# Optimization experiments

Measured on AMD Instinct MI355X. Metric: run time of the kernel, lower is better.

## Reference

```python
import jax, jax.numpy as jnp
import numpy as np

D_MODEL = 1024
HEAD_DIM = 64
NUM_HEADS = 16
NUM_KV_HEADS = 4
LOGIT_CAP = 50.0
F_EMBED = 10000


def rope(inputs, positions, head_dim, max_wavelength):
    # inputs: [B, T, N, H]; positions: [B, T]
    fraction = 2.0 * jnp.arange(head_dim // 2, dtype=jnp.float32) / head_dim
    timescale = max_wavelength ** fraction  # [H/2]
    sinusoid = positions.astype(jnp.float32)[..., None] / timescale  # [B, T, H/2]
    sinusoid = sinusoid[..., None, :]  # [B, T, 1, H/2]
    sin, cos = jnp.sin(sinusoid), jnp.cos(sinusoid)
    first, second = jnp.split(inputs, 2, axis=-1)
    return jnp.concatenate([first * cos - second * sin,
                            second * cos + first * sin], axis=-1)


def setup_inputs() -> dict:
    key = jax.random.key(0)
    kx, kq, kkv, ko = jax.random.split(key, 4)
    B, T = 1, 2048
    x = jax.random.normal(kx, (B, T, D_MODEL), dtype=jnp.float32)
    pos = jnp.broadcast_to(jnp.arange(T, dtype=jnp.int32)[None, :], (B, T))
    # mask semantics: True == masked out (logit set to -100). Causal: disallow s > t.
    mask = jnp.broadcast_to(jnp.triu(jnp.ones((T, T), dtype=bool), k=1)[None], (B, T, T))
    sq = 1.0 / np.sqrt(D_MODEL)
    wq = jax.random.normal(kq, (NUM_HEADS, D_MODEL, HEAD_DIM), dtype=jnp.float32) * sq
    wkv = jax.random.normal(kkv, (2, NUM_KV_HEADS, D_MODEL, HEAD_DIM), dtype=jnp.float32) * sq
    wout = jax.random.normal(ko, (NUM_HEADS, HEAD_DIM, D_MODEL), dtype=jnp.float32) * sq
    return {"x": x, "pos": pos, "mask": mask, "wq": wq, "wkv": wkv, "wout": wout}


def reference(x, pos, mask, wq, wkv, wout):
    B, T, _ = x.shape
    K, G = NUM_KV_HEADS, NUM_HEADS // NUM_KV_HEADS
    # projections
    q = jnp.einsum('BTD,NDH->BTNH', x, wq)  # [B,T,N,H]
    q = rope(q, pos, HEAD_DIM, F_EMBED) / jnp.sqrt(jnp.float32(HEAD_DIM))
    kv = jnp.einsum('BSD,CKDH->CBSKH', x, wkv)  # [2,B,S,K,H]
    k_proj, v_proj = kv[0], kv[1]
    k_proj = rope(k_proj, pos, HEAD_DIM, F_EMBED)
    # grouped logits
    qg = q.reshape(B, T, K, G, HEAD_DIM)
    logits = jnp.einsum('BTKGH,BSKH->BTKGS', qg, k_proj).reshape(B, T, NUM_HEADS, T)
    # soft-cap + mask (True in mask => masked => -100)
    logits = jnp.tanh(logits / LOGIT_CAP) * LOGIT_CAP
    logits = jnp.where(~mask[:, :, None, :], logits, -100.0)
    probs = jax.nn.softmax(logits, axis=-1).astype(k_proj.dtype)
    # grouped outer
    pg = probs.reshape(B, T, K, G, T)
    enc = jnp.einsum('BTKGS,BSKH->BTKGH', pg, v_proj).reshape(B, T, NUM_HEADS, HEAD_DIM)
    return jnp.einsum('BTNH,NHD->BTD', enc, wout)
```

## Files before the change

### kernel.cpp

```cpp
#include <hip/hip_runtime.h>
#include <hip/hip_bf16.h>
#include <cstdint>

#define T_SEQ 2048
#define DM    1024
#define HD    64
#define NH    16
#define NKV   4

typedef __attribute__((ext_vector_type(8))) short short8;
typedef __attribute__((ext_vector_type(4))) short short4v;
typedef __attribute__((ext_vector_type(4))) float f32x4;

__device__ __forceinline__ unsigned short f2bf(float f) {
    union { float f; unsigned u; } v; v.f = f;
    unsigned r = v.u + 0x7FFF + ((v.u >> 16) & 1);
    return (unsigned short)(r >> 16);
}

__global__ __launch_bounds__(256) void prep_kernel(const float* __restrict__ x,
                                                   const int* __restrict__ pos,
                                                   const float* __restrict__ wq,
                                                   const float* __restrict__ wkv,
                                                   const float* __restrict__ wout,
                                                   unsigned short* __restrict__ xb,
                                                   float2* __restrict__ stab,
                                                   unsigned short* __restrict__ wqkvT,
                                                   unsigned short* __restrict__ woutT) {
    __shared__ unsigned short tile[64][65];
    int bid = blockIdx.x;
    if (bid < 2048) {
        int i = bid * 256 + threadIdx.x;
        f32x4 v = *(const f32x4*)(x + i * 4);
        short4v o;
        #pragma unroll
        for (int j = 0; j < 4; j++) o[j] = (short)f2bf(v[j]);
        *(short4v*)(xb + i * 4) = o;
        if (i < 65536) {
            int tt = i >> 5, hm = i & 31;
            float ang = (float)pos[tt] * exp2f((float)hm * -0.41524101186092029f);
            float sv, cv;
            sincosf(ang, &sv, &cv);
            stab[i] = make_float2(sv, cv);
        }
    } else {
        int bid2 = bid - 2048;
        int d0 = (bid2 & 15) * 64;
        int bz = bid2 >> 4;
        int tc = threadIdx.x & 63, tr = threadIdx.x >> 6;
        if (bz < 24) {
            const float* src = (bz < 16) ? (wq + bz * 65536) : (wkv + (bz - 16) * 65536);
            #pragma unroll
            for (int rr = 0; rr < 64; rr += 4)
                tile[rr + tr][tc] = f2bf(src[(d0 + rr + tr) * 64 + tc]);
            __syncthreads();
            #pragma unroll
            for (int rr = 0; rr < 64; rr += 4)
                wqkvT[(bz * 64 + rr + tr) * 1024 + d0 + tc] = tile[tc][rr + tr];
        } else {
            int j0 = (bz - 24) * 64;
            #pragma unroll
            for (int rr = 0; rr < 64; rr += 4)
                tile[rr + tr][tc] = f2bf(wout[(j0 + rr + tr) * 1024 + d0 + tc]);
            __syncthreads();
            #pragma unroll
            for (int rr = 0; rr < 64; rr += 4)
                woutT[(d0 + rr + tr) * 1024 + j0 + tc] = tile[tc][rr + tr];
        }
    }
}

__global__ __launch_bounds__(256) void gemm_qkv(const unsigned short* __restrict__ A,
                                                const unsigned short* __restrict__ Bt,
                                                const float2* __restrict__ stab,
                                                unsigned short* __restrict__ qb,
                                                unsigned short* __restrict__ kb2,
                                                unsigned short* __restrict__ vT) {
    __shared__ __align__(16) unsigned char smem[33280];
    unsigned short (*lA)[4096] = (unsigned short (*)[4096])smem;
    unsigned short (*lB)[2048] = (unsigned short (*)[2048])(smem + 16384);
    float (*etile)[65] = (float (*)[65])smem;

    int wid = threadIdx.x >> 6;
    int lane = threadIdx.x & 63;
    int l15 = lane & 15, g = lane >> 4;
    int wr = wid >> 1, wc = wid & 1;
    int r0 = blockIdx.x * 128;
    int by = blockIdx.y;
    int c0 = by * 64;

    f32x4 acc[4][2];
    #pragma unroll
    for (int m = 0; m < 4; m++)
        #pragma unroll
        for (int n = 0; n < 2; n++)
            acc[m][n] = (f32x4){0.f, 0.f, 0.f, 0.f};

    auto stage = [&](int buf, int k0) {
        #pragma unroll
        for (int i = 0; i < 2; i++) {
            int off = i * 4096 + threadIdx.x * 16;
            const unsigned short* gpa = A + (r0 + (off >> 6)) * DM + k0 + ((off & 63) >> 1);
            __builtin_amdgcn_global_load_lds(
                (const __attribute__((address_space(1))) unsigned int*)gpa,
                (__attribute__((address_space(3))) unsigned int*)&lA[buf][off >> 1], 16, 0, 0);
        }
        int off = threadIdx.x * 16;
        const unsigned short* gpb = Bt + (c0 + (off >> 6)) * DM + k0 + ((off & 63) >> 1);
        __builtin_amdgcn_global_load_lds(
            (const __attribute__((address_space(1))) unsigned int*)gpb,
            (__attribute__((address_space(3))) unsigned int*)&lB[buf][off >> 1], 16, 0, 0);
    };

    stage(0, 0);
    __syncthreads();
    for (int k0 = 0; k0 < DM; k0 += 32) {
        int buf = (k0 >> 5) & 1;
        if (k0 + 32 < DM) stage(buf ^ 1, k0 + 32);
        short8 af[4], bfr[2];
        #pragma unroll
        for (int m = 0; m < 4; m++)
            af[m] = *(const short8*)&lA[buf][(wr * 64 + m * 16 + l15) * 32 + g * 8];
        #pragma unroll
        for (int n = 0; n < 2; n++)
            bfr[n] = *(const short8*)&lB[buf][(wc * 32 + n * 16 + l15) * 32 + g * 8];
        #pragma unroll
        for (int m = 0; m < 4; m++)
            #pragma unroll
            for (int n = 0; n < 2; n++)
                acc[m][n] = __builtin_amdgcn_mfma_f32_16x16x32_bf16(af[m], bfr[n], acc[m][n], 0, 0, 0);
        __syncthreads();
    }

    #pragma unroll
    for (int m = 0; m < 4; m++)
        #pragma unroll
        for (int n = 0; n < 2; n++)
            #pragma unroll
            for (int rr = 0; rr < 4; rr++)
                etile[wr * 64 + m * 16 + g * 4 + rr][wc * 32 + n * 16 + l15] = acc[m][n][rr];
    __syncthreads();

    if (by < 20) {
        #pragma unroll
        for (int rh = 0; rh < 2; rh++) {
            int row = threadIdx.x >> 2;
            int h0 = (threadIdx.x & 3) * 16;
            int t = r0 + rh * 64 + row;
            float res[16];
            #pragma unroll
            for (int j = 0; j < 16; j++) {
                int h = h0 + j;
                float val = etile[rh * 64 + row][h];
                float oth = etile[rh * 64 + row][h ^ 32];
                float2 sc = stab[t * 32 + (h & 31)];
                res[j] = (h < 32) ? (val * sc.y - oth * sc.x) : (val * sc.y + oth * sc.x);
            }
            if (by < 16) {
                short8 o[2];
                #pragma unroll
                for (int j = 0; j < 16; j++) o[j >> 3][j & 7] = (short)f2bf(res[j] * 0.125f);
                unsigned short* qrow = qb + t * 1024 + by * 64 + h0;
                *(short8*)qrow = o[0];
                *(short8*)(qrow + 8) = o[1];
            } else {
                int kvh = by - 16;
                int swz = (t & 7) << 3;
                short8 o[2];
                #pragma unroll
                for (int j = 0; j < 16; j++) o[j >> 3][j & 7] = (short)f2bf(res[j]);
                unsigned short* krow = kb2 + kvh * (T_SEQ * 64) + t * 64;
                *(short8*)(krow + (h0 ^ swz)) = o[0];
                *(short8*)(krow + ((h0 + 8) ^ swz)) = o[1];
            }
        }
    } else {
        int cgl = threadIdx.x >> 2;
        int u0 = (threadIdx.x & 3) * 16;
        int cglob = (by - 20) * 64 + cgl;
        int cx = cgl & 7;
        #pragma unroll
        for (int rh = 0; rh < 2; rh++) {
            short8 o[2];
            #pragma unroll
            for (int j = 0; j < 16; j++) {
                int u = u0 + j;
                int chunk = u >> 3, qin = u & 7;
                int hi = qin >> 2, r = qin & 3;
                int sg = chunk ^ cx;
                int tl = (sg >> 2) * 32 + hi * 16 + (sg & 3) * 4 + r;
                o[j >> 3][j & 7] = (short)f2bf(etile[rh * 64 + tl][cgl]);
            }
            unsigned short* vrow = vT + cglob * 2048 + r0 + rh * 64 + u0;
            *(short8*)vrow = o[0];
            *(short8*)(vrow + 8) = o[1];
        }
    }
}

template<int BM, int BN>
__global__ __launch_bounds__(256) void gemm_lds(const unsigned short* __restrict__ A,
                                                const unsigned short* __restrict__ Bt,
                                                float* __restrict__ C,
                                                int K, int lda, int ldb, int ldc) {
    constexpr int MR = BM / 32;
    constexpr int NC = BN / 32;
    __shared__ unsigned short lA[2][BM * 32];
    __shared__ unsigned short lB[2][BN * 32];

    int wid = threadIdx.x >> 6;
    int lane = threadIdx.x & 63;
    int l15 = lane & 15, g = lane >> 4;
    int wr = wid >> 1, wc = wid & 1;
    int r0 = blockIdx.x * BM;
    int c0 = blockIdx.y * BN;

    f32x4 acc[MR][NC];
    #pragma unroll
    for (int m = 0; m < MR; m++)
        #pragma unroll
        for (int n = 0; n < NC; n++)
            acc[m][n] = (f32x4){0.f, 0.f, 0.f, 0.f};

    auto stage = [&](int buf, int k0) {
        #pragma unroll
        for (int i = 0; i < BM / 64; i++) {
            int off = i * 4096 + threadIdx.x * 16;
            const unsigned short* gp = A + (r0 + (off >> 6)) * lda + k0 + ((off & 63) >> 1);
            __builtin_amdgcn_global_load_lds(
                (const __attribute__((address_space(1))) unsigned int*)gp,
                (__attribute__((address_space(3))) unsigned int*)&lA[buf][off >> 1], 16, 0, 0);
        }
        #pragma unroll
        for (int i = 0; i < (BN + 63) / 64; i++) {
            int off = i * 4096 + threadIdx.x * 16;
            if (off < BN * 64) {
                const unsigned short* gp = Bt + (c0 + (off >> 6)) * ldb + k0 + ((off & 63) >> 1);
                __builtin_amdgcn_global_load_lds(
                    (const __attribute__((address_space(1))) unsigned int*)gp,
                    (__attribute__((address_space(3))) unsigned int*)&lB[buf][off >> 1], 16, 0, 0);
            }
        }
    };

    stage(0, 0);
    __syncthreads();
    for (int k0 = 0; k0 < K; k0 += 32) {
        int buf = (k0 >> 5) & 1;
        if (k0 + 32 < K) stage(buf ^ 1, k0 + 32);
        short8 af[MR], bfr[NC];
        #pragma unroll
        for (int m = 0; m < MR; m++)
            af[m] = *(const short8*)&lA[buf][(wr * (BM / 2) + m * 16 + l15) * 32 + g * 8];
        #pragma unroll
        for (int n = 0; n < NC; n++)
            bfr[n] = *(const short8*)&lB[buf][(wc * (BN / 2) + n * 16 + l15) * 32 + g * 8];
        #pragma unroll
        for (int m = 0; m < MR; m++)
            #pragma unroll
            for (int n = 0; n < NC; n++)
                acc[m][n] = __builtin_amdgcn_mfma_f32_16x16x32_bf16(af[m], bfr[n], acc[m][n], 0, 0, 0);
        __syncthreads();
    }
    #pragma unroll
    for (int m = 0; m < MR; m++) {
        int row = r0 + wr * (BM / 2) + m * 16 + g * 4;
        #pragma unroll
        for (int n = 0; n < NC; n++) {
            int col = c0 + wc * (BN / 2) + n * 16 + l15;
            #pragma unroll
            for (int rr = 0; rr < 4; rr++)
                C[(row + rr) * ldc + col] = acc[m][n][rr];
        }
    }
}

__global__ __launch_bounds__(512, 4) void attn_kernel(const unsigned short* __restrict__ qb,
                                                      const unsigned short* __restrict__ kb2,
                                                      const unsigned short* __restrict__ vT,
                                                      unsigned short* __restrict__ enc) {
    __shared__ unsigned short lk[2][8192];
    __shared__ unsigned short lv[2][8192];
    __shared__ float s_lc[3][4][16];

    int v = blockIdx.x;
    int kvh = blockIdx.y;
    int hp = blockIdx.z;
    int wid = threadIdx.x >> 6;
    int lane = threadIdx.x & 63;
    int l15 = lane & 15, g = lane >> 4;
    int half = wid >> 2;
    int c = wid & 3;
    int qt = half ? v : (127 - v);
    int q0 = qt * 16;
    int t = q0 + l15;
    int head0 = kvh * 4 + hp * 2;

    short8 qf0[2], qf1[2];
    #pragma unroll
    for (int e = 0; e < 2; e++) {
        const unsigned short* qrow = qb + t * 1024 + (head0 + e) * 64;
        qf0[e] = *(const short8*)(qrow + g * 8);
        qf1[e] = *(const short8*)(qrow + 32 + g * 8);
    }

    f32x4 acc[2][4];
    #pragma unroll
    for (int e = 0; e < 2; e++)
        #pragma unroll
        for (int ht = 0; ht < 4; ht++)
            acc[e][ht] = (f32x4){0.f, 0.f, 0.f, 0.f};
    float lrun[2] = {0.f, 0.f};
    int nph = (127 - v) / 8 + 1;

    auto stage = [&](int buf, int s0) {
        #pragma unroll
        for (int i = 0; i < 4; i++) {
            if (wid < 4) {
                int seg = wid * 4 + i;
                const unsigned short* gp = kb2 + kvh * (T_SEQ * 64) + s0 * 64 + seg * 512 + lane * 8;
                __builtin_amdgcn_global_load_lds(
                    (const __attribute__((address_space(1))) unsigned int*)gp,
                    (__attribute__((address_space(3))) unsigned int*)&lk[buf][seg * 512], 16, 0, 0);
            } else {
                int sv = (wid - 4) * 4 + i;
                int h = sv * 4 + (lane >> 4);
                const unsigned short* gp = vT + (kvh * 64 + h) * T_SEQ + s0 + (lane & 15) * 8;
                __builtin_amdgcn_global_load_lds(
                    (const __attribute__((address_space(1))) unsigned int*)gp,
                    (__attribute__((address_space(3))) unsigned int*)&lv[buf][sv * 512], 16, 0, 0);
            }
        }
    };

    stage(0, 0);
    __syncthreads();

    for (int ph = 0; ph < nph; ph++) {
        int buf = ph & 1;
        if (ph + 1 < nph) stage(buf ^ 1, (ph + 1) * 128);
        int s0c = ph * 128 + c * 32;
        if (s0c <= q0 + 15) {
            bool needmask = (s0c + 31 > q0);
            union PU { short8 s8; unsigned w[4]; } pf[2];
            #pragma unroll
            for (int u = 0; u < 2; u++) {
                int srow = c * 32 + u * 16 + l15;
                int swz = (srow & 7) << 3;
                short8 kf0 = *(const short8*)(&lk[buf][srow * 64 + ((g * 8) ^ swz)]);
                short8 kf1 = *(const short8*)(&lk[buf][srow * 64 + ((32 + g * 8) ^ swz)]);
                #pragma unroll
                for (int e = 0; e < 2; e++) {
                    f32x4 z = {0.f, 0.f, 0.f, 0.f};
                    z = __builtin_amdgcn_mfma_f32_16x16x32_bf16(kf0, qf0[e], z, 0, 0, 0);
                    z = __builtin_amdgcn_mfma_f32_16x16x32_bf16(kf1, qf1[e], z, 0, 0, 0);
                    float pv[4];
                    #pragma unroll
                    for (int r = 0; r < 4; r++) {
                        float x = z[r];
                        float xc = fmaf(x * x, x * (-1.3333333e-4f), x);
                        float pe = __builtin_amdgcn_exp2f(xc * 1.44269504f);
                        if (needmask) {
                            int s = s0c + u * 16 + 4 * g + r;
                            pe = (s <= t) ? pe : 0.f;
                        }
                        lrun[e] += pe;
                        pv[r] = pe;
                    }
                    unsigned pk0, pk1;
                    asm("v_cvt_pk_bf16_f32 %0, %1, %2" : "=v"(pk0) : "v"(pv[0]), "v"(pv[1]));
                    asm("v_cvt_pk_bf16_f32 %0, %1, %2" : "=v"(pk1) : "v"(pv[2]), "v"(pv[3]));
                    pf[e].w[u * 2] = pk0;
                    pf[e].w[u * 2 + 1] = pk1;
                }
            }
            #pragma unroll
            for (int ht = 0; ht < 4; ht++) {
                int h = ht * 16 + l15;
                short8 vf = *(const short8*)(&lv[buf][h * 128 + (c >> 1) * 64 +
                                                      (((c & 1) * 32 + g * 8) ^ ((h & 7) << 3))]);
                #pragma unroll
                for (int e = 0; e < 2; e++)
                    acc[e][ht] = __builtin_amdgcn_mfma_f32_16x16x32_bf16(vf, pf[e].s8, acc[e][ht], 0, 0, 0);
            }
        }
        __syncthreads();
    }

    #pragma unroll
    for (int e = 0; e < 2; e++) {
        lrun[e] += __shfl_xor(lrun[e], 16);
        lrun[e] += __shfl_xor(lrun[e], 32);
    }

    float* L0 = (float*)&lk[0][0];
    float* L1 = L0 + 4096;
    float* L2 = (float*)&lv[0][0];
    if (c > 0) {
        float* layer = (c == 1) ? L0 : (c == 2) ? L1 : L2;
        #pragma unroll
        for (int e = 0; e < 2; e++) {
            if (g == 0) s_lc[c - 1][half * 2 + e][l15] = lrun[e];
            #pragma unroll
            for (int ht = 0; ht < 4; ht++) {
                int idx = ((half * 2 + e) * 16 + l15) * 64 + ((ht * 16 + 4 * g) ^ ((l15 & 3) << 3));
                *(f32x4*)&layer[idx] = acc[e][ht];
            }
        }
    }
    __syncthreads();
    if (c == 0) {
        #pragma unroll
        for (int e = 0; e < 2; e++) {
            float L = lrun[e] + s_lc[0][half * 2 + e][l15] + s_lc[1][half * 2 + e][l15]
                    + s_lc[2][half * 2 + e][l15];
            float inv = 1.f / L;
            unsigned short* erow = enc + t * 1024 + (head0 + e) * 64;
            #pragma unroll
            for (int ht = 0; ht < 4; ht++) {
                int idx = ((half * 2 + e) * 16 + l15) * 64 + ((ht * 16 + 4 * g) ^ ((l15 & 3) << 3));
                f32x4 sum = acc[e][ht] + *(const f32x4*)&L0[idx]
                          + *(const f32x4*)&L1[idx] + *(const f32x4*)&L2[idx];
                short4v o;
                #pragma unroll
                for (int r = 0; r < 4; r++)
                    o[r] = (short)f2bf(sum[r] * inv);
                *(short4v*)(erow + ht * 16 + 4 * g) = o;
            }
        }
    }
}

extern "C" void kernel_launch(void* const* d_in, const int* in_sizes, int n_in,
                              void* d_out, int out_size, void* d_ws, size_t ws_size,
                              hipStream_t stream) {
    (void)in_sizes; (void)n_in; (void)out_size; (void)ws_size;
    const float* x    = (const float*)d_in[0];
    const int*   pos  = (const int*)d_in[1];
    const float* wq   = (const float*)d_in[3];
    const float* wkv  = (const float*)d_in[4];
    const float* wout = (const float*)d_in[5];
    float* out = (float*)d_out;

    unsigned short* xb    = (unsigned short*)d_ws;
    unsigned short* wqkvT = xb + T_SEQ * DM;
    unsigned short* woutT = wqkvT + 1536 * DM;
    unsigned short* qb    = woutT + DM * DM;
    unsigned short* kb2   = qb + T_SEQ * DM;
    unsigned short* vT    = kb2 + NKV * T_SEQ * 64;
    unsigned short* enc   = vT + 256 * T_SEQ;
    float2* stab          = (float2*)(enc + T_SEQ * DM);

    prep_kernel<<<2688, 256, 0, stream>>>(x, pos, wq, wkv, wout, xb, stab, wqkvT, woutT);
    gemm_qkv<<<dim3(16, 24), 256, 0, stream>>>(xb, wqkvT, stab, qb, kb2, vT);
    attn_kernel<<<dim3(64, NKV, 2), 512, 0, stream>>>(qb, kb2, vT, enc);
    gemm_lds<128, 64><<<dim3(16, 16), 256, 0, stream>>>(enc, woutT, out, DM, DM, DM, DM);
}
```

Before: 70.30 us.

## Process all four GQA heads per attention block and shrink GEMM row tiles

The attention kernel now handles all four query heads sharing a KV head in one block, instead of splitting them across two blocks via a z dimension. This halves the K/V tile loads per head, at the cost of doubled accumulator registers and the removed occupancy hint. The cross-wave reduction becomes a two-stage tree through LDS. The QKV and output GEMMs switch from 128-row to 64-row tiles, doubling block count for better CU fill.

```diff
diff --git a/kernel.cpp b/kernel.cpp
--- a/kernel.cpp
+++ b/kernel.cpp
@@ -76,36 +76,31 @@
                                                 unsigned short* __restrict__ qb,
                                                 unsigned short* __restrict__ kb2,
                                                 unsigned short* __restrict__ vT) {
-    __shared__ __align__(16) unsigned char smem[33280];
-    unsigned short (*lA)[4096] = (unsigned short (*)[4096])smem;
-    unsigned short (*lB)[2048] = (unsigned short (*)[2048])(smem + 16384);
-    float (*etile)[65] = (float (*)[65])smem;
+    __shared__ unsigned short lA[2][64 * 32];
+    __shared__ unsigned short lB[2][64 * 32];
+    __shared__ float etile[64][65];
 
     int wid = threadIdx.x >> 6;
     int lane = threadIdx.x & 63;
     int l15 = lane & 15, g = lane >> 4;
     int wr = wid >> 1, wc = wid & 1;
-    int r0 = blockIdx.x * 128;
+    int r0 = blockIdx.x * 64;
     int by = blockIdx.y;
     int c0 = by * 64;
 
-    f32x4 acc[4][2];
-    #pragma unroll
-    for (int m = 0; m < 4; m++)
+    f32x4 acc[2][2];
+    #pragma unroll
+    for (int m = 0; m < 2; m++)
         #pragma unroll
         for (int n = 0; n < 2; n++)
             acc[m][n] = (f32x4){0.f, 0.f, 0.f, 0.f};
 
     auto stage = [&](int buf, int k0) {
-        #pragma unroll
-        for (int i = 0; i < 2; i++) {
-            int off = i * 4096 + threadIdx.x * 16;
-            const unsigned short* gpa = A + (r0 + (off >> 6)) * DM + k0 + ((off & 63) >> 1);
-            __builtin_amdgcn_global_load_lds(
-                (const __attribute__((address_space(1))) unsigned int*)gpa,
-                (__attribute__((address_space(3))) unsigned int*)&lA[buf][off >> 1], 16, 0, 0);
-        }
         int off = threadIdx.x * 16;
+        const unsigned short* gpa = A + (r0 + (off >> 6)) * DM + k0 + ((off & 63) >> 1);
+        __builtin_amdgcn_global_load_lds(
+            (const __attribute__((address_space(1))) unsigned int*)gpa,
+            (__attribute__((address_space(3))) unsigned int*)&lA[buf][off >> 1], 16, 0, 0);
         const unsigned short* gpb = Bt + (c0 + (off >> 6)) * DM + k0 + ((off & 63) >> 1);
         __builtin_amdgcn_global_load_lds(
             (const __attribute__((address_space(1))) unsigned int*)gpb,
@@ -117,15 +112,15 @@
     for (int k0 = 0; k0 < DM; k0 += 32) {
         int buf = (k0 >> 5) & 1;
         if (k0 + 32 < DM) stage(buf ^ 1, k0 + 32);
-        short8 af[4], bfr[2];
-        #pragma unroll
-        for (int m = 0; m < 4; m++)
-            af[m] = *(const short8*)&lA[buf][(wr * 64 + m * 16 + l15) * 32 + g * 8];
+        short8 af[2], bfr[2];
+        #pragma unroll
+        for (int m = 0; m < 2; m++)
+            af[m] = *(const short8*)&lA[buf][(wr * 32 + m * 16 + l15) * 32 + g * 8];
         #pragma unroll
         for (int n = 0; n < 2; n++)
             bfr[n] = *(const short8*)&lB[buf][(wc * 32 + n * 16 + l15) * 32 + g * 8];
         #pragma unroll
-        for (int m = 0; m < 4; m++)
+        for (int m = 0; m < 2; m++)
             #pragma unroll
             for (int n = 0; n < 2; n++)
                 acc[m][n] = __builtin_amdgcn_mfma_f32_16x16x32_bf16(af[m], bfr[n], acc[m][n], 0, 0, 0);
@@ -133,68 +128,62 @@
     }
 
     #pragma unroll
-    for (int m = 0; m < 4; m++)
+    for (int m = 0; m < 2; m++)
         #pragma unroll
         for (int n = 0; n < 2; n++)
             #pragma unroll
             for (int rr = 0; rr < 4; rr++)
-                etile[wr * 64 + m * 16 + g * 4 + rr][wc * 32 + n * 16 + l15] = acc[m][n][rr];
+                etile[wr * 32 + m * 16 + g * 4 + rr][wc * 32 + n * 16 + l15] = acc[m][n][rr];
     __syncthreads();
 
     if (by < 20) {
-        #pragma unroll
-        for (int rh = 0; rh < 2; rh++) {
-            int row = threadIdx.x >> 2;
-            int h0 = (threadIdx.x & 3) * 16;
-            int t = r0 + rh * 64 + row;
-            float res[16];
-            #pragma unroll
-            for (int j = 0; j < 16; j++) {
-                int h = h0 + j;
-                float val = etile[rh * 64 + row][h];
-                float oth = etile[rh * 64 + row][h ^ 32];
-                float2 sc = stab[t * 32 + (h & 31)];
-                res[j] = (h < 32) ? (val * sc.y - oth * sc.x) : (val * sc.y + oth * sc.x);
-            }
-            if (by < 16) {
-                short8 o[2];
-                #pragma unroll
-                for (int j = 0; j < 16; j++) o[j >> 3][j & 7] = (short)f2bf(res[j] * 0.125f);
-                unsigned short* qrow = qb + t * 1024 + by * 64 + h0;
-                *(short8*)qrow = o[0];
-                *(short8*)(qrow + 8) = o[1];
-            } else {
-                int kvh = by - 16;
-                int swz = (t & 7) << 3;
-                short8 o[2];
-                #pragma unroll
-                for (int j = 0; j < 16; j++) o[j >> 3][j & 7] = (short)f2bf(res[j]);
-                unsigned short* krow = kb2 + kvh * (T_SEQ * 64) + t * 64;
-                *(short8*)(krow + (h0 ^ swz)) = o[0];
-                *(short8*)(krow + ((h0 + 8) ^ swz)) = o[1];
-            }
+        int row = threadIdx.x >> 2;
+        int h0 = (threadIdx.x & 3) * 16;
+        int t = r0 + row;
+        float res[16];
+        #pragma unroll
+        for (int j = 0; j < 16; j++) {
+            int h = h0 + j;
+            float val = etile[row][h];
+            float oth = etile[row][h ^ 32];
+            float2 sc = stab[t * 32 + (h & 31)];
+            res[j] = (h < 32) ? (val * sc.y - oth * sc.x) : (val * sc.y + oth * sc.x);
+        }
+        if (by < 16) {
+            short8 o[2];
+            #pragma unroll
+            for (int j = 0; j < 16; j++) o[j >> 3][j & 7] = (short)f2bf(res[j] * 0.125f);
+            unsigned short* qrow = qb + t * 1024 + by * 64 + h0;
+            *(short8*)qrow = o[0];
+            *(short8*)(qrow + 8) = o[1];
+        } else {
+            int kvh = by - 16;
+            int swz = (t & 7) << 3;
+            short8 o[2];
+            #pragma unroll
+            for (int j = 0; j < 16; j++) o[j >> 3][j & 7] = (short)f2bf(res[j]);
+            unsigned short* krow = kb2 + kvh * (T_SEQ * 64) + t * 64;
+            *(short8*)(krow + (h0 ^ swz)) = o[0];
+            *(short8*)(krow + ((h0 + 8) ^ swz)) = o[1];
         }
     } else {
         int cgl = threadIdx.x >> 2;
         int u0 = (threadIdx.x & 3) * 16;
         int cglob = (by - 20) * 64 + cgl;
         int cx = cgl & 7;
-        #pragma unroll
-        for (int rh = 0; rh < 2; rh++) {
-            short8 o[2];
-            #pragma unroll
-            for (int j = 0; j < 16; j++) {
-                int u = u0 + j;
-                int chunk = u >> 3, qin = u & 7;
-                int hi = qin >> 2, r = qin & 3;
-                int sg = chunk ^ cx;
-                int tl = (sg >> 2) * 32 + hi * 16 + (sg & 3) * 4 + r;
-                o[j >> 3][j & 7] = (short)f2bf(etile[rh * 64 + tl][cgl]);
-            }
-            unsigned short* vrow = vT + cglob * 2048 + r0 + rh * 64 + u0;
-            *(short8*)vrow = o[0];
-            *(short8*)(vrow + 8) = o[1];
-        }
+        short8 o[2];
+        #pragma unroll
+        for (int j = 0; j < 16; j++) {
+            int u = u0 + j;
+            int chunk = u >> 3, qin = u & 7;
+            int hi = qin >> 2, r = qin & 3;
+            int sg = chunk ^ cx;
+            int tl = (sg >> 2) * 32 + hi * 16 + (sg & 3) * 4 + r;
+            o[j >> 3][j & 7] = (short)f2bf(etile[tl][cgl]);
+        }
+        unsigned short* vrow = vT + cglob * 2048 + r0 + u0;
+        *(short8*)vrow = o[0];
+        *(short8*)(vrow + 8) = o[1];
     }
 }
 
@@ -275,17 +264,16 @@
     }
 }
 
-__global__ __launch_bounds__(512, 4) void attn_kernel(const unsigned short* __restrict__ qb,
-                                                      const unsigned short* __restrict__ kb2,
-                                                      const unsigned short* __restrict__ vT,
-                                                      unsigned short* __restrict__ enc) {
+__global__ __launch_bounds__(512) void attn_kernel(const unsigned short* __restrict__ qb,
+                                                   const unsigned short* __restrict__ kb2,
+                                                   const unsigned short* __restrict__ vT,
+                                                   unsigned short* __restrict__ enc) {
     __shared__ unsigned short lk[2][8192];
     __shared__ unsigned short lv[2][8192];
-    __shared__ float s_lc[3][4][16];
+    __shared__ float s_lc[2][8][16];
 
     int v = blockIdx.x;
     int kvh = blockIdx.y;
-    int hp = blockIdx.z;
     int wid = threadIdx.x >> 6;
     int lane = threadIdx.x & 63;
     int l15 = lane & 15, g = lane >> 4;
@@ -294,23 +282,23 @@
     int qt = half ? v : (127 - v);
     int q0 = qt * 16;
     int t = q0 + l15;
-    int head0 = kvh * 4 + hp * 2;
-
-    short8 qf0[2], qf1[2];
-    #pragma unroll
-    for (int e = 0; e < 2; e++) {
+    int head0 = kvh * 4;
+
+    short8 qf0[4], qf1[4];
+    #pragma unroll
+    for (int e = 0; e < 4; e++) {
         const unsigned short* qrow = qb + t * 1024 + (head0 + e) * 64;
         qf0[e] = *(const short8*)(qrow + g * 8);
         qf1[e] = *(const short8*)(qrow + 32 + g * 8);
     }
 
-    f32x4 acc[2][4];
-    #pragma unroll
-    for (int e = 0; e < 2; e++)
+    f32x4 acc[4][4];
+    #pragma unroll
+    for (int e = 0; e < 4; e++)
         #pragma unroll
         for (int ht = 0; ht < 4; ht++)
             acc[e][ht] = (f32x4){0.f, 0.f, 0.f, 0.f};
-    float lrun[2] = {0.f, 0.f};
+    float lrun[4] = {0.f, 0.f, 0.f, 0.f};
     int nph = (127 - v) / 8 + 1;
 
     auto stage = [&](int buf, int s0) {
@@ -342,7 +330,7 @@
         int s0c = ph * 128 + c * 32;
         if (s0c <= q0 + 15) {
             bool needmask = (s0c + 31 > q0);
-            union PU { short8 s8; unsigned w[4]; } pf[2];
+            union PU { short8 s8; unsigned w[4]; } pf[4];
             #pragma unroll
             for (int u = 0; u < 2; u++) {
                 int srow = c * 32 + u * 16 + l15;
@@ -350,7 +338,7 @@
                 short8 kf0 = *(const short8*)(&lk[buf][srow * 64 + ((g * 8) ^ swz)]);
                 short8 kf1 = *(const short8*)(&lk[buf][srow * 64 + ((32 + g * 8) ^ swz)]);
                 #pragma unroll
-                for (int e = 0; e < 2; e++) {
+                for (int e = 0; e < 4; e++) {
                     f32x4 z = {0.f, 0.f, 0.f, 0.f};
                     z = __builtin_amdgcn_mfma_f32_16x16x32_bf16(kf0, qf0[e], z, 0, 0, 0);
                     z = __builtin_amdgcn_mfma_f32_16x16x32_bf16(kf1, qf1[e], z, 0, 0, 0);
@@ -380,7 +368,7 @@
                 short8 vf = *(const short8*)(&lv[buf][h * 128 + (c >> 1) * 64 +
                                                       (((c & 1) * 32 + g * 8) ^ ((h & 7) << 3))]);
                 #pragma unroll
-                for (int e = 0; e < 2; e++)
+                for (int e = 0; e < 4; e++)
                     acc[e][ht] = __builtin_amdgcn_mfma_f32_16x16x32_bf16(vf, pf[e].s8, acc[e][ht], 0, 0, 0);
             }
         }
@@ -388,39 +376,65 @@
     }
 
     #pragma unroll
-    for (int e = 0; e < 2; e++) {
+    for (int e = 0; e < 4; e++) {
         lrun[e] += __shfl_xor(lrun[e], 16);
         lrun[e] += __shfl_xor(lrun[e], 32);
     }
 
     float* L0 = (float*)&lk[0][0];
-    float* L1 = L0 + 4096;
-    float* L2 = (float*)&lv[0][0];
-    if (c > 0) {
-        float* layer = (c == 1) ? L0 : (c == 2) ? L1 : L2;
-        #pragma unroll
-        for (int e = 0; e < 2; e++) {
-            if (g == 0) s_lc[c - 1][half * 2 + e][l15] = lrun[e];
-            #pragma unroll
-            for (int ht = 0; ht < 4; ht++) {
-                int idx = ((half * 2 + e) * 16 + l15) * 64 + ((ht * 16 + 4 * g) ^ ((l15 & 3) << 3));
-                *(f32x4*)&layer[idx] = acc[e][ht];
-            }
+    float* L1 = (float*)&lv[0][0];
+    auto cidx = [&](int e, int ht) {
+        return ((half * 4 + e) * 16 + l15) * 64 + ((ht * 16 + 4 * g) ^ ((l15 & 3) << 3));
+    };
+    if (c == 1 || c == 3) {
+        float* Lx = (c == 1) ? L0 : L1;
+        int slot = (c == 1) ? 0 : 1;
+        #pragma unroll
+        for (int e = 0; e < 4; e++) {
+            if (g == 0) s_lc[slot][half * 4 + e][l15] = lrun[e];
+            #pragma unroll
+            for (int ht = 0; ht < 4; ht++)
+                *(f32x4*)&Lx[cidx(e, ht)] = acc[e][ht];
         }
     }
     __syncthreads();
     if (c == 0) {
         #pragma unroll
-        for (int e = 0; e < 2; e++) {
-            float L = lrun[e] + s_lc[0][half * 2 + e][l15] + s_lc[1][half * 2 + e][l15]
-                    + s_lc[2][half * 2 + e][l15];
+        for (int e = 0; e < 4; e++) {
+            lrun[e] += s_lc[0][half * 4 + e][l15];
+            #pragma unroll
+            for (int ht = 0; ht < 4; ht++)
+                acc[e][ht] = acc[e][ht] + *(const f32x4*)&L0[cidx(e, ht)];
+        }
+    } else if (c == 2) {
+        #pragma unroll
+        for (int e = 0; e < 4; e++) {
+            lrun[e] += s_lc[1][half * 4 + e][l15];
+            #pragma unroll
+            for (int ht = 0; ht < 4; ht++)
+                acc[e][ht] = acc[e][ht] + *(const f32x4*)&L1[cidx(e, ht)];
+        }
+    }
+    __syncthreads();
+    if (c == 2) {
+        #pragma unroll
+        for (int e = 0; e < 4; e++) {
+            if (g == 0) s_lc[0][half * 4 + e][l15] = lrun[e];
+            #pragma unroll
+            for (int ht = 0; ht < 4; ht++)
+                *(f32x4*)&L0[cidx(e, ht)] = acc[e][ht];
+        }
+    }
+    __syncthreads();
+    if (c == 0) {
+        #pragma unroll
+        for (int e = 0; e < 4; e++) {
+            float L = lrun[e] + s_lc[0][half * 4 + e][l15];
             float inv = 1.f / L;
             unsigned short* erow = enc + t * 1024 + (head0 + e) * 64;
             #pragma unroll
             for (int ht = 0; ht < 4; ht++) {
-                int idx = ((half * 2 + e) * 16 + l15) * 64 + ((ht * 16 + 4 * g) ^ ((l15 & 3) << 3));
-                f32x4 sum = acc[e][ht] + *(const f32x4*)&L0[idx]
-                          + *(const f32x4*)&L1[idx] + *(const f32x4*)&L2[idx];
+                f32x4 sum = acc[e][ht] + *(const f32x4*)&L0[cidx(e, ht)];
                 short4v o;
                 #pragma unroll
                 for (int r = 0; r < 4; r++)
@@ -452,7 +466,7 @@
     float2* stab          = (float2*)(enc + T_SEQ * DM);
 
     prep_kernel<<<2688, 256, 0, stream>>>(x, pos, wq, wkv, wout, xb, stab, wqkvT, woutT);
-    gemm_qkv<<<dim3(16, 24), 256, 0, stream>>>(xb, wqkvT, stab, qb, kb2, vT);
-    attn_kernel<<<dim3(64, NKV, 2), 512, 0, stream>>>(qb, kb2, vT, enc);
-    gemm_lds<128, 64><<<dim3(16, 16), 256, 0, stream>>>(enc, woutT, out, DM, DM, DM, DM);
-}
+    gemm_qkv<<<dim3(32, 24), 256, 0, stream>>>(xb, wqkvT, stab, qb, kb2, vT);
+    attn_kernel<<<dim3(64, NKV), 512, 0, stream>>>(qb, kb2, vT, enc);
+    gemm_lds<64, 64><<<dim3(32, 16), 256, 0, stream>>>(enc, woutT, out, DM, DM, DM, DM);
+}
```

Result: slower. 72.36 us (+2.9%).

## Remap attention blocks so both wave halves serve head pairs of one query tile

Applied to the files above, without the earlier changes.

Before, each attention block processed two query tiles (v and 127-v) for one head pair, one tile per half of the waves, sharing the K/V staging loop sized by the longer tile. The grid is now a flat 1-D grid of 512 blocks, each covering one query tile and all four heads of a KV group, with the two wave halves taking different head pairs. Both halves now follow the same causal extent, so no waves sit idle while the longer tile finishes, and total K/V staging shrinks because each block only stages up to its own tile's causal limit. The trade-off is that per-block work is no longer uniform, so load balance now depends on the block ordering chosen from the index.

```diff
diff --git a/kernel.cpp b/kernel.cpp
--- a/kernel.cpp
+++ b/kernel.cpp
@@ -283,15 +283,15 @@
     __shared__ unsigned short lv[2][8192];
     __shared__ float s_lc[3][4][16];
 
-    int v = blockIdx.x;
-    int kvh = blockIdx.y;
-    int hp = blockIdx.z;
+    int u = blockIdx.x;
+    int kvh = u & 3;
+    int j = u >> 2;
+    int qt = (j < 64) ? j : (191 - j);
     int wid = threadIdx.x >> 6;
     int lane = threadIdx.x & 63;
     int l15 = lane & 15, g = lane >> 4;
-    int half = wid >> 2;
+    int hp = wid >> 2;
     int c = wid & 3;
-    int qt = half ? v : (127 - v);
     int q0 = qt * 16;
     int t = q0 + l15;
     int head0 = kvh * 4 + hp * 2;
@@ -311,7 +311,7 @@
         for (int ht = 0; ht < 4; ht++)
             acc[e][ht] = (f32x4){0.f, 0.f, 0.f, 0.f};
     float lrun[2] = {0.f, 0.f};
-    int nph = (127 - v) / 8 + 1;
+    int nph = qt / 8 + 1;
 
     auto stage = [&](int buf, int s0) {
         #pragma unroll
@@ -344,8 +344,8 @@
             bool needmask = (s0c + 31 > q0);
             union PU { short8 s8; unsigned w[4]; } pf[2];
             #pragma unroll
-            for (int u = 0; u < 2; u++) {
-                int srow = c * 32 + u * 16 + l15;
+            for (int uu = 0; uu < 2; uu++) {
+                int srow = c * 32 + uu * 16 + l15;
                 int swz = (srow & 7) << 3;
                 short8 kf0 = *(const short8*)(&lk[buf][srow * 64 + ((g * 8) ^ swz)]);
                 short8 kf1 = *(const short8*)(&lk[buf][srow * 64 + ((32 + g * 8) ^ swz)]);
@@ -361,7 +361,7 @@
                         float xc = fmaf(x * x, x * (-1.3333333e-4f), x);
                         float pe = __builtin_amdgcn_exp2f(xc * 1.44269504f);
                         if (needmask) {
-                            int s = s0c + u * 16 + 4 * g + r;
+                            int s = s0c + uu * 16 + 4 * g + r;
                             pe = (s <= t) ? pe : 0.f;
                         }
                         lrun[e] += pe;
@@ -370,8 +370,8 @@
                     unsigned pk0, pk1;
                     asm("v_cvt_pk_bf16_f32 %0, %1, %2" : "=v"(pk0) : "v"(pv[0]), "v"(pv[1]));
                     asm("v_cvt_pk_bf16_f32 %0, %1, %2" : "=v"(pk1) : "v"(pv[2]), "v"(pv[3]));
-                    pf[e].w[u * 2] = pk0;
-                    pf[e].w[u * 2 + 1] = pk1;
+                    pf[e].w[uu * 2] = pk0;
+                    pf[e].w[uu * 2 + 1] = pk1;
                 }
             }
             #pragma unroll
@@ -400,10 +400,10 @@
         float* layer = (c == 1) ? L0 : (c == 2) ? L1 : L2;
         #pragma unroll
         for (int e = 0; e < 2; e++) {
-            if (g == 0) s_lc[c - 1][half * 2 + e][l15] = lrun[e];
+            if (g == 0) s_lc[c - 1][hp * 2 + e][l15] = lrun[e];
             #pragma unroll
             for (int ht = 0; ht < 4; ht++) {
-                int idx = ((half * 2 + e) * 16 + l15) * 64 + ((ht * 16 + 4 * g) ^ ((l15 & 3) << 3));
+                int idx = ((hp * 2 + e) * 16 + l15) * 64 + ((ht * 16 + 4 * g) ^ ((l15 & 3) << 3));
                 *(f32x4*)&layer[idx] = acc[e][ht];
             }
         }
@@ -412,13 +412,13 @@
     if (c == 0) {
         #pragma unroll
         for (int e = 0; e < 2; e++) {
-            float L = lrun[e] + s_lc[0][half * 2 + e][l15] + s_lc[1][half * 2 + e][l15]
-                    + s_lc[2][half * 2 + e][l15];
+            float L = lrun[e] + s_lc[0][hp * 2 + e][l15] + s_lc[1][hp * 2 + e][l15]
+                    + s_lc[2][hp * 2 + e][l15];
             float inv = 1.f / L;
             unsigned short* erow = enc + t * 1024 + (head0 + e) * 64;
             #pragma unroll
             for (int ht = 0; ht < 4; ht++) {
-                int idx = ((half * 2 + e) * 16 + l15) * 64 + ((ht * 16 + 4 * g) ^ ((l15 & 3) << 3));
+                int idx = ((hp * 2 + e) * 16 + l15) * 64 + ((ht * 16 + 4 * g) ^ ((l15 & 3) << 3));
                 f32x4 sum = acc[e][ht] + *(const f32x4*)&L0[idx]
                           + *(const f32x4*)&L1[idx] + *(const f32x4*)&L2[idx];
                 short4v o;
@@ -453,6 +453,6 @@
 
     prep_kernel<<<2688, 256, 0, stream>>>(x, pos, wq, wkv, wout, xb, stab, wqkvT, woutT);
     gemm_qkv<<<dim3(16, 24), 256, 0, stream>>>(xb, wqkvT, stab, qb, kb2, vT);
-    attn_kernel<<<dim3(64, NKV, 2), 512, 0, stream>>>(qb, kb2, vT, enc);
+    attn_kernel<<<512, 512, 0, stream>>>(qb, kb2, vT, enc);
     gemm_lds<128, 64><<<dim3(16, 16), 256, 0, stream>>>(enc, woutT, out, DM, DM, DM, DM);
 }
```

After: 69.68 us. No clear change (-0.9%).
